# Optimization experiments

Hardware: AMD Instinct MI355X
Metric: run time of the kernel (lower is better)

The kernel has to match this reference:

```python
import jax, jax.numpy as jnp
import numpy as np

B, N, D_IN, D_OUT, R = 8, 1024, 256, 256, 4


def setup_inputs() -> dict:
    key = jax.random.key(0)
    ks = jax.random.split(key, 8)
    scale_in = 1.0 / np.sqrt(D_IN)
    scale_out = 1.0 / np.sqrt(2 * D_OUT)
    scale_g = 1.0 / np.sqrt(D_OUT)
    return {
        "node_features": jax.random.normal(ks[0], (B, N, D_IN), dtype=jnp.float32),
        "adj_matrix": jax.random.randint(ks[1], (B, R, N, N), 0, 2, dtype=jnp.int32),
        "rel_w": jax.random.uniform(ks[2], (R, D_OUT, D_IN), jnp.float32, -scale_in, scale_in),
        "rel_b": jax.random.uniform(ks[3], (R, D_OUT), jnp.float32, -scale_in, scale_in),
        "attn_w": jax.random.uniform(ks[4], (2 * D_OUT,), jnp.float32, -scale_out, scale_out),
        "attn_b": jax.random.uniform(ks[5], (), jnp.float32, -scale_out, scale_out),
        "gate_w": jax.random.uniform(ks[6], (D_OUT,), jnp.float32, -scale_g, scale_g),
        "gate_b": jax.random.uniform(ks[7], (), jnp.float32, -scale_g, scale_g),
    }


def reference(node_features, adj_matrix, rel_w, rel_b, attn_w, attn_b, gate_w, gate_b):
    # Per-relation projections: [B, R, N, D]
    feats = jnp.einsum('bni,rdi->brnd', node_features, rel_w) + rel_b[None, :, None, :]
    # attn_proj(cat([h_i, h_j])) == h_i @ w_i + h_j @ w_j + b  (linear over concat)
    d = feats.shape[-1]
    si = jnp.einsum('brnd,d->brn', feats, attn_w[:d])   # contribution of row node i
    sj = jnp.einsum('brnd,d->brn', feats, attn_w[d:])   # contribution of col node j
    score = si[:, :, :, None] + sj[:, :, None, :] + attn_b  # [B, R, N, N]
    score = jnp.where(adj_matrix == 0, jnp.float32(-1e9), score)
    attn = jax.nn.softmax(score, axis=-1)
    # Aggregate over relations: sum_r attn_r @ feats_r -> [B, N, D]
    agg = jnp.einsum('brnm,brmd->bnd', attn, feats)
    gate = jax.nn.sigmoid(jnp.einsum('bnd,d->bn', agg, gate_w) + gate_b)
    return gate[:, :, None] * agg
```

## Files before the change

### kernel.cpp

```cpp
#include <hip/hip_runtime.h>
#include <hip/hip_bf16.h>

#define B_ 8
#define N_ 1024
#define DIN 256
#define DOUT 256
#define R_ 4

typedef __attribute__((ext_vector_type(8))) short bf16x8;
typedef __attribute__((ext_vector_type(4))) float f32x4;
typedef __attribute__((ext_vector_type(4))) int i32x4;

__device__ __forceinline__ unsigned short f2bf(float f) {
    union { float f; unsigned int u; } v; v.f = f;
    unsigned int u = v.u;
    u += 0x7fffu + ((u >> 16) & 1u);
    return (unsigned short)(u >> 16);
}

__device__ __forceinline__ void gl_lds16(const void* g, void* l) {
    __builtin_amdgcn_global_load_lds(
        (const __attribute__((address_space(1))) unsigned int*)g,
        (__attribute__((address_space(3))) unsigned int*)l, 16, 0, 0);
}

__global__ __launch_bounds__(256) void k0_swz(const float* __restrict__ rw,
                                              unsigned short* __restrict__ swzW) {
    int t = blockIdx.x * 256 + threadIdx.x;
    int lane = t & 63, nb = (t >> 6) & 15, ks = (t >> 10) & 7, r = t >> 13;
    int m = lane & 15, q = lane >> 4;
    const float* src = rw + ((r * DOUT + nb * 16 + m) * DIN) + ks * 32 + q * 8;
    float4 v0 = *(const float4*)src;
    float4 v1 = *(const float4*)(src + 4);
    bf16x8 o;
    o[0] = (short)f2bf(v0.x); o[1] = (short)f2bf(v0.y);
    o[2] = (short)f2bf(v0.z); o[3] = (short)f2bf(v0.w);
    o[4] = (short)f2bf(v1.x); o[5] = (short)f2bf(v1.y);
    o[6] = (short)f2bf(v1.z); o[7] = (short)f2bf(v1.w);
    *(bf16x8*)(swzW + (long)t * 8) = o;
}

__global__ __launch_bounds__(256) void k1_proj(const float* __restrict__ node,
        const unsigned short* __restrict__ swzW, const float* __restrict__ rel_b,
        const float* __restrict__ attn_w,
        unsigned short* __restrict__ fswz, unsigned short* __restrict__ ebf) {
    __shared__ unsigned short Wbuf[2][8192];
    int bid = blockIdx.x;
    int nt = bid & 15, r = (bid >> 4) & 3, b = bid >> 6;
    int w = threadIdx.x >> 6, lane = threadIdx.x & 63;
    int m = lane & 15, q = lane >> 4;
    int n0 = nt * 64 + w * 16;

    const float* Abase = node + ((b * N_ + n0 + m) * DIN) + q * 8;
    const unsigned short* Wsrc = swzW + r * 65536;

#pragma unroll
    for (int i = 0; i < 4; i++)
        gl_lds16(Wsrc + (w * 4 + i) * 512 + lane * 8, &Wbuf[0][(w * 4 + i) * 512]);

    f32x4 acc[16];
#pragma unroll
    for (int i = 0; i < 16; i++) acc[i] = (f32x4)0.0f;

    float4 a0 = *(const float4*)(Abase);
    float4 a1 = *(const float4*)(Abase + 4);

    for (int ks = 0; ks < 8; ks++) {
        int cur = ks & 1;
        __syncthreads();
        if (ks < 7) {
#pragma unroll
            for (int i = 0; i < 4; i++)
                gl_lds16(Wsrc + ((ks + 1) * 16 + w * 4 + i) * 512 + lane * 8,
                         &Wbuf[cur ^ 1][(w * 4 + i) * 512]);
        }
        bf16x8 af;
        af[0] = (short)f2bf(a0.x); af[1] = (short)f2bf(a0.y);
        af[2] = (short)f2bf(a0.z); af[3] = (short)f2bf(a0.w);
        af[4] = (short)f2bf(a1.x); af[5] = (short)f2bf(a1.y);
        af[6] = (short)f2bf(a1.z); af[7] = (short)f2bf(a1.w);
        if (ks < 7) {
            a0 = *(const float4*)(Abase + (ks + 1) * 32);
            a1 = *(const float4*)(Abase + (ks + 1) * 32 + 4);
        }
#pragma unroll
        for (int nb = 0; nb < 16; nb++) {
            bf16x8 wf = *(const bf16x8*)(&Wbuf[cur][nb * 512 + lane * 8]);
            acc[nb] = __builtin_amdgcn_mfma_f32_16x16x32_bf16(af, wf, acc[nb], 0, 0, 0);
        }
    }

    float sj0 = 0.f, sj1 = 0.f, sj2 = 0.f, sj3 = 0.f;
    float bias[16], aw[16];
#pragma unroll
    for (int nb = 0; nb < 16; nb++) {
        int d = nb * 16 + m;
        bias[nb] = rel_b[r * DOUT + d];
        aw[nb] = attn_w[DOUT + d];
        sj0 += (acc[nb][0] + bias[nb]) * aw[nb];
        sj1 += (acc[nb][1] + bias[nb]) * aw[nb];
        sj2 += (acc[nb][2] + bias[nb]) * aw[nb];
        sj3 += (acc[nb][3] + bias[nb]) * aw[nb];
    }
#pragma unroll
    for (int mk = 1; mk <= 8; mk <<= 1) {
        sj0 += __shfl_xor(sj0, mk, 64);
        sj1 += __shfl_xor(sj1, mk, 64);
        sj2 += __shfl_xor(sj2, mk, 64);
        sj3 += __shfl_xor(sj3, mk, 64);
    }
    float e0 = __expf(sj0), e1 = __expf(sj1), e2 = __expf(sj2), e3 = __expf(sj3);

    int slice = b * R_ + r;
    int js = n0 >> 5;
    int jhi = (n0 >> 4) & 1;
    int qp = jhi * 2 + (q >> 1);
    int jj0 = (q & 1) * 4;
    unsigned short* fb = fswz + ((long)(slice * 32 + js) * 16) * 512
                       + qp * 128 + m * 8 + jj0;
#pragma unroll
    for (int nb = 0; nb < 16; nb++) {
        ushort4 o;
        o.x = f2bf((acc[nb][0] + bias[nb]) * e0);
        o.y = f2bf((acc[nb][1] + bias[nb]) * e1);
        o.z = f2bf((acc[nb][2] + bias[nb]) * e2);
        o.w = f2bf((acc[nb][3] + bias[nb]) * e3);
        *(ushort4*)(fb + nb * 512) = o;
    }
    if (m == 0) {
        ushort4 o;
        o.x = f2bf(e0); o.y = f2bf(e1); o.z = f2bf(e2); o.w = f2bf(e3);
        *(ushort4*)(ebf + slice * N_ + n0 + q * 4) = o;
    }
}

__global__ __launch_bounds__(256, 3) void k3_attn(const int* __restrict__ adj,
        const unsigned short* __restrict__ fswz, const unsigned short* __restrict__ ebf,
        float* __restrict__ aggp) {
    __shared__ unsigned short Gbuf[2][8192];
    __shared__ int Abuf[2][2048];
    __shared__ unsigned short Ebuf[1024];

    int bid = blockIdx.x;
    int slice = (bid & 7) * 4 + ((bid >> 3) & 3);
    int it = bid >> 5;
    int t = threadIdx.x, lane = t & 63, w = t >> 6;
    int m = lane & 15, q = lane >> 4;
    int i0b = it * 64;

    const unsigned short* fsl = fswz + (size_t)slice * 262144;
    const int* adjsl = adj + (size_t)slice * (N_ * N_);
    const unsigned short* esl = ebf + slice * N_;

    int hh = lane >> 3, c = lane & 7;

#pragma unroll
    for (int i = 0; i < 4; i++)
        gl_lds16(fsl + (w * 4 + i) * 512 + lane * 8, &Gbuf[0][(w * 4 + i) * 512]);
#pragma unroll
    for (int i = 0; i < 2; i++) {
        int g = w * 2 + i;
        gl_lds16(adjsl + ((size_t)(i0b + g * 8 + hh) << 10) + ((c ^ hh) << 2),
                 &Abuf[0][g * 256]);
    }
    if (w == 0) {
        gl_lds16(esl + lane * 8, &Ebuf[0]);
        gl_lds16(esl + 512 + lane * 8, &Ebuf[512]);
    }

    f32x4 acc[16];
#pragma unroll
    for (int i = 0; i < 16; i++) acc[i] = (f32x4)0.0f;
    float l = 0.f;

    int h = m & 7;
    int gr = w * 2 + (m >> 3);

    for (int s = 0; s < 32; s++) {
        int cur = s & 1;
        __syncthreads();
        if (s < 31) {
            int ns = s + 1;
#pragma unroll
            for (int i = 0; i < 4; i++)
                gl_lds16(fsl + (size_t)ns * 8192 + (w * 4 + i) * 512 + lane * 8,
                         &Gbuf[cur ^ 1][(w * 4 + i) * 512]);
#pragma unroll
            for (int i = 0; i < 2; i++) {
                int g = w * 2 + i;
                gl_lds16(adjsl + ((size_t)(i0b + g * 8 + hh) << 10) + ns * 32
                             + ((c ^ hh) << 2),
                         &Abuf[cur ^ 1][g * 256]);
            }
        }
        const int* Ab = &Abuf[cur][gr * 256 + h * 32];
        i32x4 av0 = *(const i32x4*)(Ab + (((2 * q) ^ h) << 2));
        i32x4 av1 = *(const i32x4*)(Ab + (((2 * q + 1) ^ h) << 2));
        bf16x8 ev = *(const bf16x8*)(&Ebuf[s * 32 + q * 8]);

        int av[8] = {av0.x, av0.y, av0.z, av0.w, av1.x, av1.y, av1.z, av1.w};
        const int* ei = (const int*)&ev;
        bf16x8 af;
        int* afi = (int*)&af;
#pragma unroll
        for (int p = 0; p < 4; p++) {
            unsigned int msk = (av[2 * p] ? 0xffffu : 0u)
                             | (av[2 * p + 1] ? 0xffff0000u : 0u);
            afi[p] = (int)(msk & 0x3F803F80u);
            int me = ei[p] & (int)msk;
            union { int i; float f; } lo, hi;
            lo.i = me << 16;
            hi.i = me & (int)0xffff0000u;
            l += lo.f + hi.f;
        }
        const unsigned short* Gb = &Gbuf[cur][lane * 8];
#pragma unroll
        for (int nb = 0; nb < 16; nb++) {
            bf16x8 bfq = *(const bf16x8*)(Gb + nb * 512);
            acc[nb] = __builtin_amdgcn_mfma_f32_16x16x32_bf16(af, bfq, acc[nb], 0, 0, 0);
        }
    }

    l += __shfl_xor(l, 16, 64);
    l += __shfl_xor(l, 32, 64);
    float invl = (l > 0.f) ? 1.0f / l : 0.f;
    float invr[4];
#pragma unroll
    for (int reg = 0; reg < 4; reg++)
        invr[reg] = __shfl(invl, (lane >> 4) * 4 + reg, 64);

    int i0 = i0b + w * 16;
#pragma unroll
    for (int nb = 0; nb < 16; nb++) {
        int d = nb * 16 + m;
        float* outp = aggp + (((long)slice * N_ + i0 + q * 4)) * DOUT + d;
#pragma unroll
        for (int reg = 0; reg < 4; reg++)
            outp[reg * DOUT] = acc[nb][reg] * invr[reg];
    }
}

__global__ __launch_bounds__(256) void k4_out(const float* __restrict__ aggp,
        const float* __restrict__ gate_w, const float* __restrict__ gate_b,
        float* __restrict__ out) {
    __shared__ float red[4];
    int bid = blockIdx.x;
    int n = bid & 1023, b = bid >> 10;
    int d = threadIdx.x;
    float s = 0.f;
#pragma unroll
    for (int r = 0; r < R_; r++)
        s += aggp[(((long)(b * R_ + r) * N_) + n) * DOUT + d];
    float v = s * gate_w[d];
#pragma unroll
    for (int off = 32; off; off >>= 1) v += __shfl_down(v, off, 64);
    int lane = d & 63, wave = d >> 6;
    if (lane == 0) red[wave] = v;
    __syncthreads();
    float tot = red[0] + red[1] + red[2] + red[3];
    float g = 1.f / (1.f + __expf(-(tot + gate_b[0])));
    out[((long)(b * N_ + n)) * DOUT + d] = g * s;
}

extern "C" void kernel_launch(void* const* d_in, const int* in_sizes, int n_in,
                              void* d_out, int out_size, void* d_ws, size_t ws_size,
                              hipStream_t stream) {
    const float* node   = (const float*)d_in[0];
    const int*   adj    = (const int*)d_in[1];
    const float* rel_w  = (const float*)d_in[2];
    const float* rel_b  = (const float*)d_in[3];
    const float* attn_w = (const float*)d_in[4];
    const float* gate_w = (const float*)d_in[6];
    const float* gate_b = (const float*)d_in[7];
    float* out = (float*)d_out;

    char* ws = (char*)d_ws;
    unsigned short* swzW = (unsigned short*)ws;
    unsigned short* fswz = (unsigned short*)(ws + 524288);
    unsigned short* ebf  = (unsigned short*)(ws + 524288 + 16777216);
    float*          aggp = (float*)(ws + 524288 + 16777216 + 65536);

    k0_swz<<<128, 256, 0, stream>>>(rel_w, swzW);
    k1_proj<<<512, 256, 0, stream>>>(node, swzW, rel_b, attn_w, fswz, ebf);
    k3_attn<<<512, 256, 0, stream>>>(adj, fswz, ebf, aggp);
    k4_out<<<8192, 256, 0, stream>>>(aggp, gate_w, gate_b, out);
}
```

Baseline: 264.3 us.

## Split attention over key halves, load adjacency directly to registers, defer normalization

The attention kernel now splits the 1024 key columns into two halves, doubling the grid to 1024 blocks and raising the occupancy target to 4. Adjacency tiles are loaded straight into registers with a one-step prefetch instead of being staged through LDS, which frees shared memory. Each half writes unnormalized partial sums as bf16 plus its softmax denominator, and the output kernel combines the halves and normalizes. This adds more parallelism and lower LDS pressure, but doubles partial-result storage, makes the final kernel read twice as many partials, and adds bf16 rounding of the unnormalized accumulators.

```diff
diff --git a/kernel.cpp b/kernel.cpp
--- a/kernel.cpp
+++ b/kernel.cpp
@@ -16,6 +16,10 @@
     unsigned int u = v.u;
     u += 0x7fffu + ((u >> 16) & 1u);
     return (unsigned short)(u >> 16);
+}
+__device__ __forceinline__ float bf2f(unsigned short h) {
+    union { float f; unsigned int u; } v; v.u = ((unsigned int)h) << 16;
+    return v.f;
 }
 
 __device__ __forceinline__ void gl_lds16(const void* g, void* l) {
@@ -134,71 +138,53 @@
     }
 }
 
-__global__ __launch_bounds__(256, 3) void k3_attn(const int* __restrict__ adj,
+__global__ __launch_bounds__(256, 4) void k3_attn(const int* __restrict__ adj,
         const unsigned short* __restrict__ fswz, const unsigned short* __restrict__ ebf,
-        float* __restrict__ aggp) {
+        unsigned short* __restrict__ aggU, float* __restrict__ lbuf) {
     __shared__ unsigned short Gbuf[2][8192];
-    __shared__ int Abuf[2][2048];
-    __shared__ unsigned short Ebuf[1024];
+    __shared__ unsigned short Ebuf[512];
 
     int bid = blockIdx.x;
     int slice = (bid & 7) * 4 + ((bid >> 3) & 3);
-    int it = bid >> 5;
+    int rest = bid >> 5;
+    int it = rest & 15, jh = rest >> 4;
     int t = threadIdx.x, lane = t & 63, w = t >> 6;
     int m = lane & 15, q = lane >> 4;
     int i0b = it * 64;
 
-    const unsigned short* fsl = fswz + (size_t)slice * 262144;
-    const int* adjsl = adj + (size_t)slice * (N_ * N_);
-    const unsigned short* esl = ebf + slice * N_;
-
-    int hh = lane >> 3, c = lane & 7;
+    const unsigned short* fsl = fswz + ((size_t)(slice * 32 + jh * 16)) * 8192;
+    const int* adjbase = adj + (size_t)slice * (N_ * N_)
+                       + (size_t)(i0b + w * 16 + m) * N_ + jh * 512 + q * 8;
+    const unsigned short* esl = ebf + slice * N_ + jh * 512;
 
 #pragma unroll
     for (int i = 0; i < 4; i++)
         gl_lds16(fsl + (w * 4 + i) * 512 + lane * 8, &Gbuf[0][(w * 4 + i) * 512]);
-#pragma unroll
-    for (int i = 0; i < 2; i++) {
-        int g = w * 2 + i;
-        gl_lds16(adjsl + ((size_t)(i0b + g * 8 + hh) << 10) + ((c ^ hh) << 2),
-                 &Abuf[0][g * 256]);
-    }
-    if (w == 0) {
+    if (w == 0)
         gl_lds16(esl + lane * 8, &Ebuf[0]);
-        gl_lds16(esl + 512 + lane * 8, &Ebuf[512]);
-    }
+
+    i32x4 A0c = *(const i32x4*)(adjbase);
+    i32x4 A1c = *(const i32x4*)(adjbase + 4);
 
     f32x4 acc[16];
 #pragma unroll
     for (int i = 0; i < 16; i++) acc[i] = (f32x4)0.0f;
     float l = 0.f;
 
-    int h = m & 7;
-    int gr = w * 2 + (m >> 3);
-
-    for (int s = 0; s < 32; s++) {
+    for (int s = 0; s < 16; s++) {
         int cur = s & 1;
         __syncthreads();
-        if (s < 31) {
-            int ns = s + 1;
+        i32x4 A0n, A1n;
+        if (s < 15) {
 #pragma unroll
             for (int i = 0; i < 4; i++)
-                gl_lds16(fsl + (size_t)ns * 8192 + (w * 4 + i) * 512 + lane * 8,
+                gl_lds16(fsl + (size_t)(s + 1) * 8192 + (w * 4 + i) * 512 + lane * 8,
                          &Gbuf[cur ^ 1][(w * 4 + i) * 512]);
-#pragma unroll
-            for (int i = 0; i < 2; i++) {
-                int g = w * 2 + i;
-                gl_lds16(adjsl + ((size_t)(i0b + g * 8 + hh) << 10) + ns * 32
-                             + ((c ^ hh) << 2),
-                         &Abuf[cur ^ 1][g * 256]);
-            }
-        }
-        const int* Ab = &Abuf[cur][gr * 256 + h * 32];
-        i32x4 av0 = *(const i32x4*)(Ab + (((2 * q) ^ h) << 2));
-        i32x4 av1 = *(const i32x4*)(Ab + (((2 * q + 1) ^ h) << 2));
+            A0n = *(const i32x4*)(adjbase + (s + 1) * 32);
+            A1n = *(const i32x4*)(adjbase + (s + 1) * 32 + 4);
+        }
         bf16x8 ev = *(const bf16x8*)(&Ebuf[s * 32 + q * 8]);
-
-        int av[8] = {av0.x, av0.y, av0.z, av0.w, av1.x, av1.y, av1.z, av1.w};
+        int av[8] = {A0c.x, A0c.y, A0c.z, A0c.w, A1c.x, A1c.y, A1c.z, A1c.w};
         const int* ei = (const int*)&ev;
         bf16x8 af;
         int* afi = (int*)&af;
@@ -219,38 +205,41 @@
             bf16x8 bfq = *(const bf16x8*)(Gb + nb * 512);
             acc[nb] = __builtin_amdgcn_mfma_f32_16x16x32_bf16(af, bfq, acc[nb], 0, 0, 0);
         }
+        A0c = A0n; A1c = A1n;
     }
 
     l += __shfl_xor(l, 16, 64);
     l += __shfl_xor(l, 32, 64);
-    float invl = (l > 0.f) ? 1.0f / l : 0.f;
-    float invr[4];
-#pragma unroll
-    for (int reg = 0; reg < 4; reg++)
-        invr[reg] = __shfl(invl, (lane >> 4) * 4 + reg, 64);
-
-    int i0 = i0b + w * 16;
+    int half = slice * 2 + jh;
+    if (lane < 16)
+        lbuf[half * N_ + i0b + w * 16 + lane] = l;
+
+    unsigned short* ob = aggU + ((size_t)half * N_ + i0b + w * 16 + q * 4) * DOUT + m;
 #pragma unroll
     for (int nb = 0; nb < 16; nb++) {
-        int d = nb * 16 + m;
-        float* outp = aggp + (((long)slice * N_ + i0 + q * 4)) * DOUT + d;
 #pragma unroll
         for (int reg = 0; reg < 4; reg++)
-            outp[reg * DOUT] = acc[nb][reg] * invr[reg];
-    }
-}
-
-__global__ __launch_bounds__(256) void k4_out(const float* __restrict__ aggp,
-        const float* __restrict__ gate_w, const float* __restrict__ gate_b,
-        float* __restrict__ out) {
+            ob[(size_t)reg * DOUT + nb * 16] = f2bf(acc[nb][reg]);
+    }
+}
+
+__global__ __launch_bounds__(256) void k4_out(const unsigned short* __restrict__ aggU,
+        const float* __restrict__ lbuf, const float* __restrict__ gate_w,
+        const float* __restrict__ gate_b, float* __restrict__ out) {
     __shared__ float red[4];
     int bid = blockIdx.x;
     int n = bid & 1023, b = bid >> 10;
     int d = threadIdx.x;
     float s = 0.f;
 #pragma unroll
-    for (int r = 0; r < R_; r++)
-        s += aggp[(((long)(b * R_ + r) * N_) + n) * DOUT + d];
+    for (int r = 0; r < R_; r++) {
+        int sl = b * R_ + r;
+        float a0 = bf2f(aggU[((size_t)(sl * 2 + 0) * N_ + n) * DOUT + d]);
+        float a1 = bf2f(aggU[((size_t)(sl * 2 + 1) * N_ + n) * DOUT + d]);
+        float lt = lbuf[(sl * 2 + 0) * N_ + n] + lbuf[(sl * 2 + 1) * N_ + n];
+        float inv = (lt > 0.f) ? 1.0f / lt : 0.f;
+        s += (a0 + a1) * inv;
+    }
     float v = s * gate_w[d];
 #pragma unroll
     for (int off = 32; off; off >>= 1) v += __shfl_down(v, off, 64);
@@ -277,11 +266,12 @@
     char* ws = (char*)d_ws;
     unsigned short* swzW = (unsigned short*)ws;
     unsigned short* fswz = (unsigned short*)(ws + 524288);
-    unsigned short* ebf  = (unsigned short*)(ws + 524288 + 16777216);
-    float*          aggp = (float*)(ws + 524288 + 16777216 + 65536);
+    unsigned short* ebf  = (unsigned short*)(ws + 17301504);
+    unsigned short* aggU = (unsigned short*)(ws + 17367040);
+    float*          lbuf = (float*)(ws + 50921472);
 
     k0_swz<<<128, 256, 0, stream>>>(rel_w, swzW);
     k1_proj<<<512, 256, 0, stream>>>(node, swzW, rel_b, attn_w, fswz, ebf);
-    k3_attn<<<512, 256, 0, stream>>>(adj, fswz, ebf, aggp);
-    k4_out<<<8192, 256, 0, stream>>>(aggp, gate_w, gate_b, out);
-}
+    k3_attn<<<1024, 256, 0, stream>>>(adj, fswz, ebf, aggU, lbuf);
+    k4_out<<<8192, 256, 0, stream>>>(aggU, lbuf, gate_w, gate_b, out);
+}
```

Measured after the change: 252.6 us. 1.05x faster.
